# Performance work log

Hardware: AMD Instinct MI355X
Metric: run time of the kernel (lower is better)

Reference implementation:

```python
import jax, jax.numpy as jnp
import numpy as np

B, T, H, V, L = 16, 256, 512, 32, 2


def setup_inputs() -> dict:
    key = jax.random.key(0)
    ks = jax.random.split(key, 24)
    s = 1.0 / np.sqrt(H)
    d = {}
    d["encoder_outputs"] = jax.random.normal(ks[0], (B, T, H), jnp.float32)
    d["h0"] = jax.random.normal(ks[1], (L, B, H), jnp.float32)
    d["c0"] = jax.random.normal(ks[2], (L, B, H), jnp.float32)
    d["audio_lengths"] = jax.random.randint(ks[3], (B,), 1, T + 1, jnp.int32)
    d["Wq"] = jax.random.normal(ks[4], (H, H), jnp.float32) * s
    d["bq"] = jnp.zeros((H,), jnp.float32)
    d["Wk"] = jax.random.normal(ks[5], (H, H), jnp.float32) * s
    d["bk"] = jnp.zeros((H,), jnp.float32)
    d["v"] = jax.random.normal(ks[6], (H,), jnp.float32) * s
    d["vb"] = jnp.zeros((1,), jnp.float32)
    d["Wih0"] = jax.random.normal(ks[7], (4 * H, 2 * H), jnp.float32) * s
    d["bih0"] = jnp.zeros((4 * H,), jnp.float32)
    d["Whh0"] = jax.random.normal(ks[8], (4 * H, H), jnp.float32) * s
    d["bhh0"] = jnp.zeros((4 * H,), jnp.float32)
    d["Wih1"] = jax.random.normal(ks[9], (4 * H, H), jnp.float32) * s
    d["bih1"] = jnp.zeros((4 * H,), jnp.float32)
    d["Whh1"] = jax.random.normal(ks[10], (4 * H, H), jnp.float32) * s
    d["bhh1"] = jnp.zeros((4 * H,), jnp.float32)
    d["Wout"] = jax.random.normal(ks[11], (V, H), jnp.float32) * s
    d["bout"] = jnp.zeros((V,), jnp.float32)
    return d


def _lstm_cell(x, h, c, Wih, bih, Whh, bhh):
    # PyTorch gate order: i, f, g, o
    g = x @ Wih.T + bih + h @ Whh.T + bhh
    i, f, gg, o = jnp.split(g, 4, axis=-1)
    c2 = jax.nn.sigmoid(f) * c + jax.nn.sigmoid(i) * jnp.tanh(gg)
    h2 = jax.nn.sigmoid(o) * jnp.tanh(c2)
    return h2, c2


def reference(encoder_outputs, h0, c0, audio_lengths, Wq, bq, Wk, bk, v, vb,
              Wih0, bih0, Whh0, bhh0, Wih1, bih1, Whh1, bhh1, Wout, bout):
    # Precompute key projection once (same math as per-step Wk @ keys)
    Kproj = encoder_outputs @ Wk.T + bk  # [B,T,H]

    def step(carry, enc_t):
        h, c = carry  # each [L,B,H]
        q = h[-1]  # [B,H] top-layer hidden drives attention
        e = jnp.tanh((q @ Wq.T + bq)[:, None, :] + Kproj)  # [B,T,H]
        scores = jnp.einsum('bth,h->bt', e, v) + vb[0]  # [B,T]
        w = jax.nn.softmax(scores, axis=-1)
        ctx = jnp.einsum('bt,bth->bh', w, encoder_outputs)  # [B,H]
        x = jnp.concatenate([enc_t, ctx], axis=-1)  # [B,2H]
        h0n, c0n = _lstm_cell(x, h[0], c[0], Wih0, bih0, Whh0, bhh0)
        h1n, c1n = _lstm_cell(h0n, h[1], c[1], Wih1, bih1, Whh1, bhh1)
        logit = h1n @ Wout.T + bout  # [B,V]
        return (jnp.stack([h0n, h1n]), jnp.stack([c0n, c1n])), logit

    _, logits = jax.lax.scan(step, (h0, c0), jnp.swapaxes(encoder_outputs, 0, 1))
    return jnp.swapaxes(logits, 0, 1)  # [B,T,V]
```

## Files before the change

kernel.cpp:

```cpp
#include <hip/hip_runtime.h>

#define HH 512
#define BB 16
#define TT 256
#define VV 32
#define TPB 512
#define NBLK 256
#define PITCH 516

#define BAR_INTS 512

typedef unsigned long long ull;

struct KArgs {
  const float* enc; const float* h0in; const float* c0in;
  const float* Wq; const float* bq; const float* vatt; const float* vb;
  const float* Wih0; const float* bih0; const float* Whh0; const float* bhh0;
  const float* Wih1; const float* bih1; const float* Whh1; const float* bhh1;
  const float* Wout; const float* bout;
  const float* Kproj; ull* H0tag; float* H1buf; ull* qWtag; float* Ug; float* Zg;
  int* bar; float* out;
};

struct Smem {
  float W0e[4][2][PITCH];
  float W0c[4][2][PITCH];
  float W0h[4][2][PITCH];
  float W1x[4][2][PITCH];
  float W1h[4][2][PITCH];
  float Wqr[2][PITCH];
  float Wor[2][PITCH];
  float vv[HH];
  union { float qrow[HH]; float red[8][64]; } qr;
  float stg[BB][PITCH];
  float pre0[BB][4][2];
  float pre1[BB][4][2];
  float cst[2][2][BB];
  float scw[16];
  float zinv[BB];
  float bs0[4][2];
  float bs1[4][2];
  float bqv[2], boutv[2];
};

__device__ __forceinline__ float fsig(float x){ return 1.0f/(1.0f + __expf(-x)); }
__device__ __forceinline__ float ftanh(float x){
  float ee = __expf(2.0f*x);
  return 1.0f - 2.0f/(ee + 1.0f);
}

__device__ __forceinline__ void stcc(float* p, float v){
  __hip_atomic_store(p, v, __ATOMIC_RELAXED, __HIP_MEMORY_SCOPE_AGENT);
}
__device__ __forceinline__ float ldcc(const float* p){
  return __hip_atomic_load(p, __ATOMIC_RELAXED, __HIP_MEMORY_SCOPE_AGENT);
}
__device__ __forceinline__ float2 ld2cc(const float* p){
  ull v = __hip_atomic_load((const ull*)p, __ATOMIC_RELAXED, __HIP_MEMORY_SCOPE_AGENT);
  union { ull u; float2 f; } c; c.u = v;
  return c.f;
}

__device__ __forceinline__ ull  ppack(float v, int tag){
  return (ull)(unsigned)__float_as_int(v) | ((ull)(unsigned)tag << 32);
}
__device__ __forceinline__ float pval(ull x){ return __int_as_float((int)(unsigned)x); }
__device__ __forceinline__ int   ptag(ull x){ return (int)(unsigned)(x >> 32); }
__device__ __forceinline__ void st_pair(ull* p, float v, int tag){
  __hip_atomic_store(p, ppack(v, tag), __ATOMIC_RELAXED, __HIP_MEMORY_SCOPE_AGENT);
}
__device__ __forceinline__ ull ld_pair(const ull* p){
  return __hip_atomic_load(p, __ATOMIC_RELAXED, __HIP_MEMORY_SCOPE_AGENT);
}

__device__ __forceinline__ void ldbuf_cc(const float* __restrict__ src,
                                         float2* __restrict__ v, int tid){
  #pragma unroll
  for (int it = 0; it < 8; ++it)
    v[it] = ld2cc(&src[(it*TPB + tid)*2]);
}
__device__ __forceinline__ void stg_regs(const float2* __restrict__ v,
                                         float (* __restrict__ stg)[PITCH], int tid){
  #pragma unroll
  for (int it = 0; it < 8; ++it){
    const int i2 = (it*TPB + tid)*2;
    *(float2*)&stg[i2 >> 9][i2 & 511] = v[it];
  }
}

__device__ __forceinline__ void poll_stage16(const ull* __restrict__ r, int exptag,
                                             float (* __restrict__ stg)[PITCH], int tid){
  int spins = 0;
  for (;;){
    int ok = 1;
    #pragma unroll
    for (int it = 0; it < 16; ++it){
      const int idx = it*TPB + tid;
      const ull v = ld_pair(&r[idx]);
      ok &= (ptag(v) == exptag);
      stg[idx >> 9][idx & 511] = pval(v);
    }
    if (ok) break;
    __builtin_amdgcn_s_sleep(1);
    if (++spins > (1 << 20)) break;
  }
}

__device__ __forceinline__ void gbar_arrive(int* __restrict__ bar, int e, int bid){
  __syncthreads();
  if (threadIdx.x == 0)
    __hip_atomic_store(&bar[bid], e, __ATOMIC_RELAXED, __HIP_MEMORY_SCOPE_AGENT);
}
__device__ __forceinline__ void gbar_wait(int* __restrict__ bar, int e, int bid){
  if (threadIdx.x < 64){
    const ull* p = (const ull*)bar;
    const int i0 = threadIdx.x * 2;
    int spins = 0;
    for (;;){
      ull v0 = __hip_atomic_load(&p[i0],     __ATOMIC_RELAXED, __HIP_MEMORY_SCOPE_AGENT);
      ull v1 = __hip_atomic_load(&p[i0 + 1], __ATOMIC_RELAXED, __HIP_MEMORY_SCOPE_AGENT);
      const int a0 = (int)v0, a1 = (int)(v0 >> 32), a2 = (int)v1, a3 = (int)(v1 >> 32);
      const int ok = (a0 >= e) & (a1 >= e) & (a2 >= e) & (a3 >= e);
      if (__all(ok)) break;
      __builtin_amdgcn_s_sleep(1);
      if (++spins > (1 << 20)) break;
    }
  }
  __syncthreads();
}

__device__ __forceinline__ void gbar2(int* __restrict__ bar2, int et, int bid, int ba){
  __syncthreads();
  if (threadIdx.x == 0)
    __hip_atomic_store(&bar2[bid], et, __ATOMIC_RELAXED, __HIP_MEMORY_SCOPE_AGENT);
  if (threadIdx.x < 64){
    const ull* p = (const ull*)bar2 + ba*8;
    int spins = 0;
    for (;;){
      int ok = 1;
      if (threadIdx.x < 8){
        ull v = __hip_atomic_load(&p[threadIdx.x], __ATOMIC_RELAXED, __HIP_MEMORY_SCOPE_AGENT);
        ok = ((int)v >= et) & ((int)(v >> 32) >= et);
      }
      if (__all(ok)) break;
      __builtin_amdgcn_s_sleep(1);
      if (++spins > (1 << 20)) break;
    }
  }
  __syncthreads();
}

__device__ __forceinline__ void dot8(const float* __restrict__ W,
                                     const float (* __restrict__ stg)[PITCH],
                                     float (* __restrict__ red)[64],
                                     int wave, int lane){
  const int jj = wave >> 2, off = (wave & 3) << 7;
  const int b = lane & 15, g = lane >> 4;
  const float* wrow = W + (size_t)(g*2 + jj)*PITCH + off;
  const float* xrow = &stg[b][off];
  float a0 = 0.f, a1 = 0.f, a2 = 0.f, a3 = 0.f;
  #pragma unroll
  for (int h = 0; h < 128; h += 16){
    const float4 w0 = *(const float4*)&wrow[h];      const float4 x0 = *(const float4*)&xrow[h];
    const float4 w1 = *(const float4*)&wrow[h + 4];  const float4 x1 = *(const float4*)&xrow[h + 4];
    const float4 w2 = *(const float4*)&wrow[h + 8];  const float4 x2 = *(const float4*)&xrow[h + 8];
    const float4 w3 = *(const float4*)&wrow[h + 12]; const float4 x3 = *(const float4*)&xrow[h + 12];
    a0 = fmaf(w0.x,x0.x, fmaf(w0.y,x0.y, fmaf(w0.z,x0.z, fmaf(w0.w,x0.w, a0))));
    a1 = fmaf(w1.x,x1.x, fmaf(w1.y,x1.y, fmaf(w1.z,x1.z, fmaf(w1.w,x1.w, a1))));
    a2 = fmaf(w2.x,x2.x, fmaf(w2.y,x2.y, fmaf(w2.z,x2.z, fmaf(w2.w,x2.w, a2))));
    a3 = fmaf(w3.x,x3.x, fmaf(w3.y,x3.y, fmaf(w3.z,x3.z, fmaf(w3.w,x3.w, a3))));
  }
  red[wave][lane] = (a0 + a1) + (a2 + a3);
}

__global__ void init_kernel(const float* __restrict__ h0in, ull* __restrict__ H0tag,
                            float* __restrict__ H1buf, ull* __restrict__ qWtag,
                            float* __restrict__ Ug, float* __restrict__ Zg,
                            int* __restrict__ bar){
  const int i = blockIdx.x*blockDim.x + threadIdx.x;
  if (i < BB*HH){
    H0tag[i] = ppack(h0in[i], 0);
    H1buf[i] = h0in[BB*HH + i];
    qWtag[i] = ppack(0.f, 0);
  }
  if (i < 2*BB*HH) Ug[i] = 0.0f;
  if (i < 32) Zg[i] = 0.0f;
  if (i < BAR_INTS) bar[i] = 0;
}

__global__ __launch_bounds__(256, 1) void kproj_kernel(const float* __restrict__ enc,
                                                       const float* __restrict__ Wk,
                                                       const float* __restrict__ bk,
                                                       float* __restrict__ Kproj){
  __shared__ float er[BB][PITCH];
  const int bid = blockIdx.x, tid = threadIdx.x;
  const int wave = tid >> 6, lane = tid & 63;
  const int r = lane & 15, q = lane >> 4;
  const int row0 = bid*16;
  #pragma unroll
  for (int it = 0; it < 8; ++it){
    const int idx = (it*256 + tid)*4;
    const int rr = idx >> 9, h = idx & 511;
    *(float4*)&er[rr][h] = *(const float4*)&enc[(size_t)(row0+rr)*HH + h];
  }
  __syncthreads();
  float4 xr[32];
  #pragma unroll
  for (int i = 0; i < 32; ++i) xr[i] = *(const float4*)&er[r][q*128 + i*4];
  for (int k = 0; k < 128; ++k){
    const int hk = wave*128 + k;
    const float* wrow = Wk + (size_t)hk*HH + q*128;
    float acc = 0.f;
    #pragma unroll
    for (int i = 0; i < 32; ++i){
      const float4 w4 = *(const float4*)&wrow[i*4];
      acc = fmaf(w4.x,xr[i].x, fmaf(w4.y,xr[i].y, fmaf(w4.z,xr[i].z, fmaf(w4.w,xr[i].w, acc))));
    }
    acc += __shfl_xor(acc, 16);
    acc += __shfl_xor(acc, 32);
    if (lane < 16) Kproj[(size_t)(row0 + r)*HH + hk] = acc + bk[hk];
  }
}

__global__ __launch_bounds__(TPB, 1) void decoder_persist(KArgs a){
  __shared__ Smem S;
  const int bid = blockIdx.x, tid = threadIdx.x;
  const int wave = tid >> 6, lane = tid & 63;
  const int lb = lane & 15, lg = lane >> 4;
  const int j0 = bid*2;
  const int ba = bid >> 4, tb = (bid & 15) * 16;
  int* bar2 = a.bar + 256;

  for (int g = 0; g < 4; ++g){
    for (int jj = 0; jj < 2; ++jj){
      const int row = g*HH + j0 + jj;
      for (int h = tid; h < HH; h += TPB){
        S.W0e[g][jj][h] = a.Wih0[(size_t)row*(2*HH) + h];
        S.W0c[g][jj][h] = a.Wih0[(size_t)row*(2*HH) + HH + h];
        S.W0h[g][jj][h] = a.Whh0[(size_t)row*HH + h];
        S.W1x[g][jj][h] = a.Wih1[(size_t)row*HH + h];
        S.W1h[g][jj][h] = a.Whh1[(size_t)row*HH + h];
      }
    }
  }
  for (int jj = 0; jj < 2; ++jj){
    const int d = bid*2 + jj, vo = d & 31;
    for (int h = tid; h < HH; h += TPB){
      S.Wqr[jj][h] = a.Wq[(size_t)(j0+jj)*HH + h];
      S.Wor[jj][h] = a.Wout[(size_t)vo*HH + h];
    }
  }
  for (int h = tid; h < HH; h += TPB) S.vv[h] = a.vatt[h];
  if (tid < 16){
    S.cst[0][0][tid] = a.c0in[0*BB*HH + tid*HH + j0];
    S.cst[0][1][tid] = a.c0in[0*BB*HH + tid*HH + j0 + 1];
    S.cst[1][0][tid] = a.c0in[1*BB*HH + tid*HH + j0];
    S.cst[1][1][tid] = a.c0in[1*BB*HH + tid*HH + j0 + 1];
  }
  if (tid < 8){
    const int g = tid & 3, jj = tid >> 2;
    const int row = g*HH + j0 + jj;
    S.bs0[g][jj] = a.bih0[row] + a.bhh0[row];
    S.bs1[g][jj] = a.bih1[row] + a.bhh1[row];
  }
  if (tid < 2){
    S.bqv[tid] = a.bq[j0 + tid];
    S.boutv[tid] = a.bout[(bid*2 + tid) & 31];
  }
  const float vb0 = a.vb[0];

  float r_kp[2][8];
  #pragma unroll
  for (int i = 0; i < 2; ++i){
    const float* kp = a.Kproj + (size_t)(ba*TT + tb + wave*2 + i)*HH;
    #pragma unroll
    for (int k = 0; k < 8; ++k) r_kp[i][k] = kp[lane + 64*k];
  }
  float r_e[16];
  #pragma unroll
  for (int lt = 0; lt < 16; ++lt)
    r_e[lt] = a.enc[(size_t)(ba*TT + tb + lt)*HH + tid];
  float4 r_en[4];
  #pragma unroll
  for (int it = 0; it < 4; ++it){
    const int idx = (it*TPB + tid)*4;
    r_en[it] = *(const float4*)&a.enc[(size_t)((idx >> 9)*TT + 0)*HH + (idx & 511)];
  }
  __syncthreads();

  {
    #pragma unroll
    for (int it = 0; it < 4; ++it){
      const int idx = (it*TPB + tid)*4;
      *(float4*)&S.stg[idx >> 9][idx & 511] = *(const float4*)&a.h0in[idx];
    }
    __syncthreads();
    dot8(&S.W0h[0][0][0], S.stg, S.qr.red, wave, lane);
    __syncthreads();
    if (tid < 128){
      const int jj = tid >> 6, l = tid & 63, g = l >> 4, b = l & 15;
      S.pre0[b][g][jj] = (S.qr.red[jj*4+0][l] + S.qr.red[jj*4+1][l])
                       + (S.qr.red[jj*4+2][l] + S.qr.red[jj*4+3][l]) + S.bs0[g][jj];
    }
    __syncthreads();
  }

  int e = 0;
  for (int t = 0; t < TT; ++t){
    const int par = t & 1, parn = par ^ 1;

    float2 r_h1[8];
    ldbuf_cc(a.H1buf + par*(BB*HH), r_h1, tid);
    stg_regs(r_h1, S.stg, tid);
    __syncthreads();

    if (wave < 2){
      if (t > 0){
        const int d = bid*2 + wave, bo = d >> 5, vo = d & 31;
        float acc = 0.f;
        #pragma unroll
        for (int k = 0; k < 8; ++k){
          const int h = lane + 64*k;
          acc = fmaf(S.Wor[wave][h], S.stg[bo][h], acc);
        }
        #pragma unroll
        for (int off = 32; off; off >>= 1) acc += __shfl_xor(acc, off);
        if (lane == 0) a.out[(size_t)(bo*TT + (t-1))*VV + vo] = acc + S.boutv[wave];
      }
    } else if (wave < 4){
      const int jj = wave - 2;
      const int off0 = lg * 128;
      float a0 = 0.f, a1 = 0.f;
      #pragma unroll
      for (int h = 0; h < 128; h += 8){
        const float4 w0 = *(const float4*)&S.Wqr[jj][off0 + h];
        const float4 x0 = *(const float4*)&S.stg[lb][off0 + h];
        const float4 w1 = *(const float4*)&S.Wqr[jj][off0 + h + 4];
        const float4 x1 = *(const float4*)&S.stg[lb][off0 + h + 4];
        a0 = fmaf(w0.x,x0.x, fmaf(w0.y,x0.y, fmaf(w0.z,x0.z, fmaf(w0.w,x0.w, a0))));
        a1 = fmaf(w1.x,x1.x, fmaf(w1.y,x1.y, fmaf(w1.z,x1.z, fmaf(w1.w,x1.w, a1))));
      }
      float acc = a0 + a1;
      acc += __shfl_xor(acc, 16);
      acc += __shfl_xor(acc, 32);
      if (lane < 16)
        st_pair(&a.qWtag[lane*HH + j0 + jj], acc + S.bqv[jj], t + 1);
    }

    dot8(&S.W1h[0][0][0], S.stg, S.qr.red, wave, lane);
    __syncthreads();
    if (tid < 128){
      const int jj = tid >> 6, l = tid & 63, g = l >> 4, b = l & 15;
      S.pre1[b][g][jj] = (S.qr.red[jj*4+0][l] + S.qr.red[jj*4+1][l])
                       + (S.qr.red[jj*4+2][l] + S.qr.red[jj*4+3][l]) + S.bs1[g][jj];
    }
    #pragma unroll
    for (int it = 0; it < 4; ++it){
      const int idx = (it*TPB + tid)*4;
      *(float4*)&S.stg[idx >> 9][idx & 511] = r_en[it];
    }
    __syncthreads();
    dot8(&S.W0e[0][0][0], S.stg, S.qr.red, wave, lane);
    __syncthreads();
    if (tid < 128){
      const int jj = tid >> 6, l = tid & 63, g = l >> 4, b = l & 15;
      S.pre0[b][g][jj] += (S.qr.red[jj*4+0][l] + S.qr.red[jj*4+1][l])
                        + (S.qr.red[jj*4+2][l] + S.qr.red[jj*4+3][l]);
    }
    __syncthreads();

    {
      float* Up = a.Ug + par*(BB*HH);
      float* Zp = a.Zg + par*16;
      {
        const ull* q = a.qWtag + ba*HH;
        int spins = 0;
        for (;;){
          const ull v = ld_pair(&q[tid]);
          if (ptag(v) == t + 1){ S.qr.qrow[tid] = pval(v); break; }
          __builtin_amdgcn_s_sleep(1);
          if (++spins > (1 << 20)) break;
        }
      }
      __syncthreads();
      #pragma unroll
      for (int i = 0; i < 2; ++i){
        float acc = 0.f;
        #pragma unroll
        for (int k = 0; k < 8; ++k){
          const int h = lane + 64*k;
          acc = fmaf(S.vv[h], ftanh(S.qr.qrow[h] + r_kp[i][k]), acc);
        }
        #pragma unroll
        for (int off = 32; off; off >>= 1) acc += __shfl_xor(acc, off);
        if (lane == 0) S.scw[wave*2 + i] = __expf(acc + vb0);
      }
      __syncthreads();
      float u = 0.f;
      #pragma unroll
      for (int lt = 0; lt < 16; ++lt)
        u = fmaf(S.scw[lt], r_e[lt], u);
      unsafeAtomicAdd(&Up[ba*HH + tid], u);
      if (tid == 0){
        float zs = 0.f;
        #pragma unroll
        for (int lt = 0; lt < 16; ++lt) zs += S.scw[lt];
        unsafeAtomicAdd(&Zp[ba], zs);
      }
    }
    gbar2(bar2, t + 1, bid, ba);

    {
      float2 r_u[8];
      ldbuf_cc(a.Ug + par*(BB*HH), r_u, tid);
      if (tid < 16) S.zinv[tid] = 1.0f / ldcc(&a.Zg[par*16 + tid]);
      stg_regs(r_u, S.stg, tid);
      __syncthreads();
      dot8(&S.W0c[0][0][0], S.stg, S.qr.red, wave, lane);
      __syncthreads();
      if (tid < 32){
        const int b = tid & 15, jj = tid >> 4;
        const float zi = S.zinv[b];
        float gv[4];
        #pragma unroll
        for (int g = 0; g < 4; ++g){
          const int l = g*16 + b;
          gv[g] = S.pre0[b][g][jj]
                + ((S.qr.red[jj*4+0][l] + S.qr.red[jj*4+1][l])
                 + (S.qr.red[jj*4+2][l] + S.qr.red[jj*4+3][l])) * zi;
        }
        const float cold = S.cst[0][jj][b];
        const float ii = fsig(gv[0]), ff = fsig(gv[1]);
        const float gg = ftanh(gv[2]), oo = fsig(gv[3]);
        const float cn = ff*cold + ii*gg;
        S.cst[0][jj][b] = cn;
        st_pair(&a.H0tag[b*HH + j0 + jj], oo * ftanh(cn), t + 1);
      }
    }

    {
      const int tn = (t + 1 < TT) ? (t + 1) : t;
      #pragma unroll
      for (int it = 0; it < 4; ++it){
        const int idx = (it*TPB + tid)*4;
        r_en[it] = *(const float4*)&a.enc[(size_t)((idx >> 9)*TT + tn)*HH + (idx & 511)];
      }
    }

    {
      if (tid < 32) stcc(&a.Ug[parn*(BB*HH) + bid*32 + tid], 0.0f);
      if (bid == 0 && tid < 16) stcc(&a.Zg[parn*16 + tid], 0.0f);

      poll_stage16(a.H0tag, t + 1, S.stg, tid);
      __syncthreads();
      dot8(&S.W1x[0][0][0], S.stg, S.qr.red, wave, lane);
      __syncthreads();
      if (tid < 32){
        const int b = tid & 15, jj = tid >> 4;
        float gv[4];
        #pragma unroll
        for (int g = 0; g < 4; ++g){
          const int l = g*16 + b;
          gv[g] = S.pre1[b][g][jj]
                + (S.qr.red[jj*4+0][l] + S.qr.red[jj*4+1][l])
                + (S.qr.red[jj*4+2][l] + S.qr.red[jj*4+3][l]);
        }
        const float cold = S.cst[1][jj][b];
        const float ii = fsig(gv[0]), ff = fsig(gv[1]);
        const float gg = ftanh(gv[2]), oo = fsig(gv[3]);
        const float cn = ff*cold + ii*gg;
        S.cst[1][jj][b] = cn;
        stcc(&a.H1buf[parn*(BB*HH) + b*HH + j0 + jj], oo * ftanh(cn));
      }
    }
    e++; gbar_arrive(a.bar, e, bid);
    {
      dot8(&S.W0h[0][0][0], S.stg, S.qr.red, wave, lane);
      __syncthreads();
      if (tid < 128){
        const int jj = tid >> 6, l = tid & 63, g = l >> 4, b = l & 15;
        S.pre0[b][g][jj] = (S.qr.red[jj*4+0][l] + S.qr.red[jj*4+1][l])
                         + (S.qr.red[jj*4+2][l] + S.qr.red[jj*4+3][l]) + S.bs0[g][jj];
      }
    }
    gbar_wait(a.bar, e, bid);
  }

  {
    float2 r_x[8];
    ldbuf_cc(a.H1buf, r_x, tid);
    stg_regs(r_x, S.stg, tid);
    __syncthreads();
    if (wave < 2){
      const int d = bid*2 + wave, bo = d >> 5, vo = d & 31;
      float acc = 0.f;
      #pragma unroll
      for (int k = 0; k < 8; ++k){
        const int h = lane + 64*k;
        acc = fmaf(S.Wor[wave][h], S.stg[bo][h], acc);
      }
      #pragma unroll
      for (int off = 32; off; off >>= 1) acc += __shfl_xor(acc, off);
      if (lane == 0) a.out[(size_t)(bo*TT + 255)*VV + vo] = acc + S.boutv[wave];
    }
  }
}

extern "C" void kernel_launch(void* const* d_in, const int* in_sizes, int n_in,
                              void* d_out, int out_size, void* d_ws, size_t ws_size,
                              hipStream_t stream){
  const float* enc  = (const float*)d_in[0];
  const float* h0in = (const float*)d_in[1];
  const float* c0in = (const float*)d_in[2];
  const float* Wq   = (const float*)d_in[4];
  const float* bq   = (const float*)d_in[5];
  const float* Wk   = (const float*)d_in[6];
  const float* bk   = (const float*)d_in[7];
  const float* vatt = (const float*)d_in[8];
  const float* vb   = (const float*)d_in[9];
  const float* Wih0 = (const float*)d_in[10];
  const float* bih0 = (const float*)d_in[11];
  const float* Whh0 = (const float*)d_in[12];
  const float* bhh0 = (const float*)d_in[13];
  const float* Wih1 = (const float*)d_in[14];
  const float* bih1 = (const float*)d_in[15];
  const float* Whh1 = (const float*)d_in[16];
  const float* bhh1 = (const float*)d_in[17];
  const float* Wout = (const float*)d_in[18];
  const float* bout = (const float*)d_in[19];

  float* ws    = (float*)d_ws;
  float* Kproj = ws;
  ull*   H0tag = (ull*)(Kproj + (size_t)BB*TT*HH);
  float* H1buf = (float*)(H0tag + BB*HH);
  ull*   qWtag = (ull*)(H1buf + 2*BB*HH);
  float* Ug    = (float*)(qWtag + BB*HH);
  float* Zg    = Ug + 2*BB*HH;
  int*   bar   = (int*)(Zg + 32);

  hipLaunchKernelGGL(init_kernel, dim3(64), dim3(256), 0, stream,
                     h0in, H0tag, H1buf, qWtag, Ug, Zg, bar);
  hipLaunchKernelGGL(kproj_kernel, dim3(256), dim3(256), 0, stream, enc, Wk, bk, Kproj);

  KArgs ka;
  ka.enc = enc; ka.h0in = h0in; ka.c0in = c0in;
  ka.Wq = Wq; ka.bq = bq; ka.vatt = vatt; ka.vb = vb;
  ka.Wih0 = Wih0; ka.bih0 = bih0; ka.Whh0 = Whh0; ka.bhh0 = bhh0;
  ka.Wih1 = Wih1; ka.bih1 = bih1; ka.Whh1 = Whh1; ka.bhh1 = bhh1;
  ka.Wout = Wout; ka.bout = bout;
  ka.Kproj = Kproj; ka.H0tag = H0tag; ka.H1buf = H1buf; ka.qWtag = qWtag;
  ka.Ug = Ug; ka.Zg = Zg; ka.bar = bar; ka.out = (float*)d_out;

  void* params[] = { (void*)&ka };
  hipLaunchCooperativeKernel((const void*)decoder_persist, dim3(NBLK), dim3(TPB),
                             params, 0, stream);
}
```

Baseline: 5.845 ms.

## Replace tagged H0 polling with double-buffered plain stores and grid barrier

Result: faster. 4.770 ms (-18.4%).

```diff
diff --git a/kernel.cpp b/kernel.cpp
--- a/kernel.cpp
+++ b/kernel.cpp
@@ -18,7 +18,7 @@
   const float* Wih0; const float* bih0; const float* Whh0; const float* bhh0;
   const float* Wih1; const float* bih1; const float* Whh1; const float* bhh1;
   const float* Wout; const float* bout;
-  const float* Kproj; ull* H0tag; float* H1buf; ull* qWtag; float* Ug; float* Zg;
+  const float* Kproj; float* H0buf; float* H1buf; ull* qWtag; float* Ug; float* Zg;
   int* bar; float* out;
 };
 
@@ -88,24 +88,6 @@
   }
 }
 
-__device__ __forceinline__ void poll_stage16(const ull* __restrict__ r, int exptag,
-                                             float (* __restrict__ stg)[PITCH], int tid){
-  int spins = 0;
-  for (;;){
-    int ok = 1;
-    #pragma unroll
-    for (int it = 0; it < 16; ++it){
-      const int idx = it*TPB + tid;
-      const ull v = ld_pair(&r[idx]);
-      ok &= (ptag(v) == exptag);
-      stg[idx >> 9][idx & 511] = pval(v);
-    }
-    if (ok) break;
-    __builtin_amdgcn_s_sleep(1);
-    if (++spins > (1 << 20)) break;
-  }
-}
-
 __device__ __forceinline__ void gbar_arrive(int* __restrict__ bar, int e, int bid){
   __syncthreads();
   if (threadIdx.x == 0)
@@ -122,7 +104,7 @@
       const int a0 = (int)v0, a1 = (int)(v0 >> 32), a2 = (int)v1, a3 = (int)(v1 >> 32);
       const int ok = (a0 >= e) & (a1 >= e) & (a2 >= e) & (a3 >= e);
       if (__all(ok)) break;
-      __builtin_amdgcn_s_sleep(1);
+      __builtin_amdgcn_s_sleep(2);
       if (++spins > (1 << 20)) break;
     }
   }
@@ -173,13 +155,13 @@
   red[wave][lane] = (a0 + a1) + (a2 + a3);
 }
 
-__global__ void init_kernel(const float* __restrict__ h0in, ull* __restrict__ H0tag,
+__global__ void init_kernel(const float* __restrict__ h0in, float* __restrict__ H0buf,
                             float* __restrict__ H1buf, ull* __restrict__ qWtag,
                             float* __restrict__ Ug, float* __restrict__ Zg,
                             int* __restrict__ bar){
   const int i = blockIdx.x*blockDim.x + threadIdx.x;
   if (i < BB*HH){
-    H0tag[i] = ppack(h0in[i], 0);
+    H0buf[i] = h0in[i];
     H1buf[i] = h0in[BB*HH + i];
     qWtag[i] = ppack(0.f, 0);
   }
@@ -434,10 +416,10 @@
         const float gg = ftanh(gv[2]), oo = fsig(gv[3]);
         const float cn = ff*cold + ii*gg;
         S.cst[0][jj][b] = cn;
-        st_pair(&a.H0tag[b*HH + j0 + jj], oo * ftanh(cn), t + 1);
-      }
-    }
-
+        stcc(&a.H0buf[parn*(BB*HH) + b*HH + j0 + jj], oo * ftanh(cn));
+      }
+    }
+    e++; gbar_arrive(a.bar, e, bid);
     {
       const int tn = (t + 1 < TT) ? (t + 1) : t;
       #pragma unroll
@@ -446,12 +428,15 @@
         r_en[it] = *(const float4*)&a.enc[(size_t)((idx >> 9)*TT + tn)*HH + (idx & 511)];
       }
     }
+    gbar_wait(a.bar, e, bid);
 
     {
       if (tid < 32) stcc(&a.Ug[parn*(BB*HH) + bid*32 + tid], 0.0f);
       if (bid == 0 && tid < 16) stcc(&a.Zg[parn*16 + tid], 0.0f);
 
-      poll_stage16(a.H0tag, t + 1, S.stg, tid);
+      float2 r_x[8];
+      ldbuf_cc(a.H0buf + parn*(BB*HH), r_x, tid);
+      stg_regs(r_x, S.stg, tid);
       __syncthreads();
       dot8(&S.W1x[0][0][0], S.stg, S.qr.red, wave, lane);
       __syncthreads();
@@ -531,15 +516,15 @@
 
   float* ws    = (float*)d_ws;
   float* Kproj = ws;
-  ull*   H0tag = (ull*)(Kproj + (size_t)BB*TT*HH);
-  float* H1buf = (float*)(H0tag + BB*HH);
+  float* H0buf = Kproj + (size_t)BB*TT*HH;
+  float* H1buf = H0buf + 2*BB*HH;
   ull*   qWtag = (ull*)(H1buf + 2*BB*HH);
   float* Ug    = (float*)(qWtag + BB*HH);
   float* Zg    = Ug + 2*BB*HH;
   int*   bar   = (int*)(Zg + 32);
 
   hipLaunchKernelGGL(init_kernel, dim3(64), dim3(256), 0, stream,
-                     h0in, H0tag, H1buf, qWtag, Ug, Zg, bar);
+                     h0in, H0buf, H1buf, qWtag, Ug, Zg, bar);
   hipLaunchKernelGGL(kproj_kernel, dim3(256), dim3(256), 0, stream, enc, Wk, bk, Kproj);
 
   KArgs ka;
@@ -548,7 +533,7 @@
   ka.Wih0 = Wih0; ka.bih0 = bih0; ka.Whh0 = Whh0; ka.bhh0 = bhh0;
   ka.Wih1 = Wih1; ka.bih1 = bih1; ka.Whh1 = Whh1; ka.bhh1 = bhh1;
   ka.Wout = Wout; ka.bout = bout;
-  ka.Kproj = Kproj; ka.H0tag = H0tag; ka.H1buf = H1buf; ka.qWtag = qWtag;
+  ka.Kproj = Kproj; ka.H0buf = H0buf; ka.H1buf = H1buf; ka.qWtag = qWtag;
   ka.Ug = Ug; ka.Zg = Zg; ka.bar = bar; ka.out = (float*)d_out;
 
   void* params[] = { (void*)&ka };
```
